# Optimization experiments

Hardware: AMD Instinct MI355X
Metric: run time of the kernel (lower is better)

Reference implementation:

```python
import jax, jax.numpy as jnp
import numpy as np

# dims: batch, time points, control channels (input_path_dim+1), cde state, mlp width
B, T, C, S, H = 64, 256, 16, 64, 128

# Tsit5 explicit tableau (5th-order solution weights; FSAL 7th stage has b7=0 and is skipped)
A21 = 0.161
A31, A32 = -0.008480655492356989, 0.335480655492357
A41, A42, A43 = 2.8971530571054935, -6.359448489975075, 4.3622954328695815
A51, A52, A53, A54 = 5.325864828439257, -11.748883564062828, 7.4955393428898365, -0.09249506636175525
A61, A62, A63, A64, A65 = 5.86145544294642, -12.92096931784711, 8.159367898576159, -0.071584973281401, -0.028269050394068383
C2, C3, C4, C5 = 0.161, 0.327, 0.9, 0.9800255409045097
BW = (0.09646076681806523, 0.01, 0.4798896504144996, 1.379008574103742, -3.290069515436081, 2.324710524099774)


def _mlp(x, ws, bs, final_act):
    for w, b in zip(ws[:-1], bs[:-1]):
        x = jax.nn.softplus(x @ w.T + b)
    return final_act(x @ ws[-1].T + bs[-1])


def _from_6d(v):  # (..., 6) -> (..., 3, 3) via Gram-Schmidt (Zhou et al. 6D rotation rep)
    a1, a2 = v[..., :3], v[..., 3:]
    b1 = a1 / jnp.linalg.norm(a1, axis=-1, keepdims=True)
    a2p = a2 - jnp.sum(b1 * a2, axis=-1, keepdims=True) * b1
    b2 = a2p / jnp.linalg.norm(a2p, axis=-1, keepdims=True)
    b3 = jnp.cross(b1, b2)
    return jnp.stack([b1, b2, b3], axis=-1)


def setup_inputs() -> dict:
    key = jax.random.key(0)
    ks = jax.random.split(key, 8)

    def lin(k, fan_in, fan_out):  # equinox Linear init: U(-1/sqrt(in), 1/sqrt(in))
        k1, k2 = jax.random.split(k)
        lim = 1.0 / np.sqrt(fan_in)
        w = jax.random.uniform(k1, (fan_out, fan_in), minval=-lim, maxval=lim, dtype=jnp.float32)
        b = jax.random.uniform(k2, (fan_out,), minval=-lim, maxval=lim, dtype=jnp.float32)
        return w, b

    ic_w0, ic_b0 = lin(ks[0], C, H)
    ic_w1, ic_b1 = lin(ks[1], H, H)
    ic_w2, ic_b2 = lin(ks[2], H, S)
    vf_w0, vf_b0 = lin(ks[3], S, H)
    vf_w1, vf_b1 = lin(ks[4], H, H)
    vf_w2, vf_b2 = lin(ks[5], H, S * C)
    ro_w, ro_b = lin(ks[6], S, 6)
    control_values = jax.random.normal(ks[7], (B, T, C), dtype=jnp.float32)
    return dict(control_values=control_values,
                ic_w0=ic_w0, ic_b0=ic_b0, ic_w1=ic_w1, ic_b1=ic_b1, ic_w2=ic_w2, ic_b2=ic_b2,
                vf_w0=vf_w0, vf_b0=vf_b0, vf_w1=vf_w1, vf_b1=vf_b1, vf_w2=vf_w2, vf_b2=vf_b2,
                ro_w=ro_w, ro_b=ro_b)


def reference(control_values, ic_w0, ic_b0, ic_w1, ic_b1, ic_w2, ic_b2,
              vf_w0, vf_b0, vf_w1, vf_b1, vf_w2, vf_b2, ro_w, ro_b):
    b, t, c = control_values.shape
    s = ic_w2.shape[0]
    h = 1.0 / (t - 1)  # uniform ts = linspace(0, 1, T)
    xs = control_values
    # backward-Hermite derivatives: d[i] = (x[i]-x[i-1])/h, d[0] = d[1]
    d = jnp.diff(xs, axis=1) / h                       # (B, T-1, C)
    dfull = jnp.concatenate([d[:, :1], d], axis=1)     # (B, T, C)

    ic_ws, ic_bs = [ic_w0, ic_w1, ic_w2], [ic_b0, ic_b1, ic_b2]
    vf_ws, vf_bs = [vf_w0, vf_w1, vf_w2], [vf_b0, vf_b1, vf_b2]

    y0 = _mlp(xs[:, 0], ic_ws, ic_bs, lambda x: x)     # (B, S)

    def vf_mat(y):  # (B, S) -> (B, S, C)
        return _mlp(y, vf_ws, vf_bs, jnp.tanh).reshape(b, s, c)

    def step(y, iv):
        yi, yip1, di, dip1 = iv  # each (B, C): interval endpoints & Hermite derivs

        def dXdt(sc):  # derivative of cubic Hermite at local coord sc in [0,1]
            s2 = sc * sc
            return (((6 * s2 - 6 * sc) / h) * yi + (3 * s2 - 4 * sc + 1) * di
                    + ((6 * sc - 6 * s2) / h) * yip1 + (3 * s2 - 2 * sc) * dip1)

        def f(yy, sc):
            return jnp.einsum('bsc,bc->bs', vf_mat(yy), dXdt(sc))

        k1 = f(y, 0.0)
        k2 = f(y + h * (A21 * k1), C2)
        k3 = f(y + h * (A31 * k1 + A32 * k2), C3)
        k4 = f(y + h * (A41 * k1 + A42 * k2 + A43 * k3), C4)
        k5 = f(y + h * (A51 * k1 + A52 * k2 + A53 * k3 + A54 * k4), C5)
        k6 = f(y + h * (A61 * k1 + A62 * k2 + A63 * k3 + A64 * k4 + A65 * k5), 1.0)
        yn = y + h * (BW[0] * k1 + BW[1] * k2 + BW[2] * k3 + BW[3] * k4 + BW[4] * k5 + BW[5] * k6)
        return yn, yn

    ivs = (jnp.swapaxes(xs[:, :-1], 0, 1), jnp.swapaxes(xs[:, 1:], 0, 1),
           jnp.swapaxes(dfull[:, :-1], 0, 1), jnp.swapaxes(dfull[:, 1:], 0, 1))
    _, ys = jax.lax.scan(step, y0, ivs)                # (T-1, B, S)
    hidden = jnp.swapaxes(jnp.concatenate([y0[None], ys], axis=0), 0, 1)  # (B, T, S)

    out6 = hidden @ ro_w.T + ro_b                      # (B, T, 6); identity readout activation
    return _from_6d(out6)                              # (B, T, 3, 3)
```

## Files before the change

### kernel.cpp

```cpp
#include <hip/hip_runtime.h>


typedef float float4v __attribute__((ext_vector_type(4)));
typedef float float2v __attribute__((ext_vector_type(2)));

__device__ __forceinline__ float dot4(float4v a, float4v b) {
  return a.x * b.x + a.y * b.y + a.z * b.z + a.w * b.w;
}

__device__ __forceinline__ float softplus_fast(float x) {
  float z = __expf(-fabsf(x));
  return fmaxf(x, 0.f) + __logf(1.f + z);
}

__device__ __forceinline__ float tanh_hw(float x) {
  float e = __expf(2.f * x);
  return 1.f - 2.f * __builtin_amdgcn_rcpf(e + 1.f);
}

__global__ __attribute__((amdgpu_waves_per_eu(2, 2)))
__launch_bounds__(512, 1) void cde_main(
    const float* __restrict__ xs,
    const float* __restrict__ icw0, const float* __restrict__ icb0,
    const float* __restrict__ icw1, const float* __restrict__ icb1,
    const float* __restrict__ icw2, const float* __restrict__ icb2,
    const float* __restrict__ vfw0, const float* __restrict__ vfb0,
    const float* __restrict__ vfw1, const float* __restrict__ vfb1,
    const float* __restrict__ vfw2, const float* __restrict__ vfb2,
    float* __restrict__ ybuf) {
  constexpr float Ac[6][5] = {
      {0.f, 0.f, 0.f, 0.f, 0.f},
      {0.161f, 0.f, 0.f, 0.f, 0.f},
      {-0.008480655492356989f, 0.335480655492357f, 0.f, 0.f, 0.f},
      {2.8971530571054935f, -6.359448489975075f, 4.3622954328695815f, 0.f, 0.f},
      {5.325864828439257f, -11.748883564062828f, 7.4955393428898365f,
       -0.09249506636175525f, 0.f},
      {5.86145544294642f, -12.92096931784711f, 8.159367898576159f,
       -0.071584973281401f, -0.028269050394068383f}};
  constexpr float SCv[6] = {0.f, 0.161f, 0.327f, 0.9f, 0.9800255409045097f, 1.f};
  constexpr float BWv[6] = {0.09646076681806523f, 0.01f, 0.4798896504144996f,
                            1.379008574103742f, -3.290069515436081f,
                            2.324710524099774f};

  const int tid = threadIdx.x;
  const int w = tid >> 6, l = tid & 63;
  const int b = blockIdx.x;

  __shared__ float sW2t[38][1024];
  __shared__ __align__(16) float sYtw[8][64];
  __shared__ __align__(16) float sH1[128];
  __shared__ __align__(16) float sH2[128];
  __shared__ float sK[6][64];

  for (int i = tid; i < 38 * 1024; i += 512) {
    int k = i >> 10, r = i & 1023;
    sW2t[k][r] = vfw2[(size_t)r * 128 + 90 + k];
  }

  const int r0 = tid * 2, r1 = r0 + 1;
  float w2a[72], w2b[72];
  {
    const float4v* p0 = (const float4v*)(vfw2 + (size_t)r0 * 128);
    const float4v* p1 = (const float4v*)(vfw2 + (size_t)r1 * 128);
#pragma unroll
    for (int kk = 0; kk < 18; ++kk) {
      float4v a = p0[kk], c = p1[kk];
      w2a[4 * kk + 0] = a.x; w2a[4 * kk + 1] = a.y;
      w2a[4 * kk + 2] = a.z; w2a[4 * kk + 3] = a.w;
      w2b[4 * kk + 0] = c.x; w2b[4 * kk + 1] = c.y;
      w2b[4 * kk + 2] = c.z; w2b[4 * kk + 3] = c.w;
    }
  }
#pragma unroll
  for (int kk = 0; kk < 72; ++kk)
    asm volatile("" : "+v"(w2a[kk]), "+v"(w2b[kk]));

  const int ii = tid >> 2, q4 = tid & 3;
  float w0r[16], w1r[32];
  {
    const float4v* p = (const float4v*)(vfw0 + (size_t)ii * 64 + q4 * 16);
#pragma unroll
    for (int kk = 0; kk < 4; ++kk) {
      float4v a = p[kk];
      w0r[4 * kk] = a.x; w0r[4 * kk + 1] = a.y;
      w0r[4 * kk + 2] = a.z; w0r[4 * kk + 3] = a.w;
    }
  }
  {
    const float4v* p = (const float4v*)(vfw1 + (size_t)ii * 128 + q4 * 32);
#pragma unroll
    for (int kk = 0; kk < 8; ++kk) {
      float4v a = p[kk];
      w1r[4 * kk] = a.x; w1r[4 * kk + 1] = a.y;
      w1r[4 * kk + 2] = a.z; w1r[4 * kk + 3] = a.w;
    }
  }
#pragma unroll
  for (int kk = 0; kk < 16; ++kk) asm volatile("" : "+v"(w0r[kk]));
#pragma unroll
  for (int kk = 0; kk < 32; ++kk) asm volatile("" : "+v"(w1r[kk]));

  const float b2r0 = vfb2[r0], b2r1 = vfb2[r1];
  const int c0 = (2 * l) & 15;
  const float b0i = vfb0[ii], b1i = vfb1[ii];

  const float* Xb = xs + (size_t)b * 4096;
  float* yb = ybuf + (size_t)b * 16384;

  __syncthreads();

  float* sTA = &sK[0][0];
  float* sTB = sH1;
  if (tid < 128) {
    float a = icb0[tid];
    const float* wr = icw0 + tid * 16;
#pragma unroll
    for (int k = 0; k < 16; ++k) a += wr[k] * Xb[k];
    sTA[tid] = softplus_fast(a);
  }
  __syncthreads();
  if (tid < 128) {
    float a = icb1[tid];
    const float* wr = icw1 + tid * 128;
    for (int k = 0; k < 128; ++k) a += wr[k] * sTA[k];
    sTB[tid] = softplus_fast(a);
  }
  __syncthreads();
  if (tid < 64) {
    float a = icb2[tid];
    const float* wr = icw2 + tid * 128;
    for (int k = 0; k < 128; ++k) a += wr[k] * sTB[k];
    sH2[tid] = a;
  }
  __syncthreads();
  float yreg = sH2[l];
  if (w == 0) yb[l] = yreg;

  const float hstep = 1.f / 255.f;
  const float invh = 255.f;

#pragma unroll 1
  for (int t = 0; t < 255; ++t) {
    float2v xt = *(const float2v*)(Xb + t * 16 + c0);
    float2v xt1 = *(const float2v*)(Xb + (t + 1) * 16 + c0);
    float2v xtm = xt;
    if (t != 0) xtm = *(const float2v*)(Xb + (t - 1) * 16 + c0);
    const float u0 = xt.x - xt1.x, u1 = xt.y - xt1.y;
    const float dp0 = (xt1.x - xt.x) * invh;
    const float dp1 = (xt1.y - xt.y) * invh;
    float di0 = (t == 0) ? dp0 : (xt.x - xtm.x) * invh;
    float di1 = (t == 0) ? dp1 : (xt.y - xtm.y) * invh;
#pragma unroll 1
    for (int j = 0; j < 6; ++j) {
      const float* wr0 = vfw2 + (size_t)r0 * 128;
      const float* wr1 = vfw2 + (size_t)r1 * 128;
      float4v sa0 = *(const float4v*)(wr0 + 72);
      float4v sa1 = *(const float4v*)(wr0 + 76);
      float4v sa2 = *(const float4v*)(wr0 + 80);
      float4v sa3 = *(const float4v*)(wr0 + 84);
      float2v sa4 = *(const float2v*)(wr0 + 88);
      float4v sb0 = *(const float4v*)(wr1 + 72);
      float4v sb1 = *(const float4v*)(wr1 + 76);
      float4v sb2 = *(const float4v*)(wr1 + 80);
      float4v sb3 = *(const float4v*)(wr1 + 84);
      float2v sb4 = *(const float2v*)(wr1 + 88);
      {
        float yt = yreg;
#pragma unroll
        for (int m = 0; m < 5; ++m)
          if (m < j) yt += hstep * Ac[j][m] * sK[m][l];
        sYtw[w][l] = yt;
      }
      asm volatile("s_waitcnt lgkmcnt(0)" ::: "memory");
      const float sc = SCv[j], s2 = sc * sc;
      const float a1 = (6.f * s2 - 6.f * sc) * invh;
      const float a2 = 3.f * s2 - 4.f * sc + 1.f;
      const float a3 = 3.f * s2 - 2.f * sc;
      const float dx0 = a1 * u0 + a2 * di0 + a3 * dp0;
      const float dx1 = a1 * u1 + a2 * di1 + a3 * dp1;
      {
        const float4v* yv = (const float4v*)(&sYtw[w][0] + q4 * 16);
        float4v y0 = yv[0], y1 = yv[1], y2 = yv[2], y3 = yv[3];
        float s = w0r[0] * y0.x + w0r[1] * y0.y + w0r[2] * y0.z +
                  w0r[3] * y0.w + w0r[4] * y1.x + w0r[5] * y1.y +
                  w0r[6] * y1.z + w0r[7] * y1.w + w0r[8] * y2.x +
                  w0r[9] * y2.y + w0r[10] * y2.z + w0r[11] * y2.w +
                  w0r[12] * y3.x + w0r[13] * y3.y + w0r[14] * y3.z +
                  w0r[15] * y3.w;
        s += __shfl_xor(s, 1);
        s += __shfl_xor(s, 2);
        if (q4 == 0) sH1[ii] = softplus_fast(s + b0i);
      }
      __syncthreads();
      {
        const float4v* hv = (const float4v*)(sH1 + q4 * 32);
        float s = 0.f;
#pragma unroll
        for (int kk = 0; kk < 8; ++kk) {
          float4v h = hv[kk];
          s += w1r[4 * kk] * h.x + w1r[4 * kk + 1] * h.y +
               w1r[4 * kk + 2] * h.z + w1r[4 * kk + 3] * h.w;
        }
        s += __shfl_xor(s, 1);
        s += __shfl_xor(s, 2);
        if (q4 == 0) sH2[ii] = softplus_fast(s + b1i);
      }
      __syncthreads();
      {
        const float4v* hv = (const float4v*)sH2;
        float s0 = 0.f, s1 = 0.f;
#pragma unroll
        for (int kk = 0; kk < 18; ++kk) {
          float4v h = hv[kk];
          s0 += w2a[4 * kk] * h.x + w2a[4 * kk + 1] * h.y +
                w2a[4 * kk + 2] * h.z + w2a[4 * kk + 3] * h.w;
          s1 += w2b[4 * kk] * h.x + w2b[4 * kk + 1] * h.y +
                w2b[4 * kk + 2] * h.z + w2b[4 * kk + 3] * h.w;
        }
        {
          float4v h0 = hv[18], h1 = hv[19], h2 = hv[20], h3 = hv[21];
          float2v h4 = *(const float2v*)(sH2 + 88);
          s0 += dot4(sa0, h0) + dot4(sa1, h1) + dot4(sa2, h2) +
                dot4(sa3, h3) + sa4.x * h4.x + sa4.y * h4.y;
          s1 += dot4(sb0, h0) + dot4(sb1, h1) + dot4(sb2, h2) +
                dot4(sb3, h3) + sb4.x * h4.x + sb4.y * h4.y;
        }
#pragma unroll 4
        for (int k2 = 0; k2 < 19; ++k2) {
          float2v hk = *(const float2v*)(sH2 + 90 + 2 * k2);
          float2v wlo = *(const float2v*)&sW2t[2 * k2][r0];
          float2v whi = *(const float2v*)&sW2t[2 * k2 + 1][r0];
          s0 += wlo.x * hk.x + whi.x * hk.y;
          s1 += wlo.y * hk.x + whi.y * hk.y;
        }
        float f = tanh_hw(s0 + b2r0) * dx0 + tanh_hw(s1 + b2r1) * dx1;
        f += __shfl_xor(f, 1);
        f += __shfl_xor(f, 2);
        f += __shfl_xor(f, 4);
        if ((tid & 7) == 0) sK[j][tid >> 3] = f;
      }
      __syncthreads();
    }
    {
      float yn = yreg;
#pragma unroll
      for (int m = 0; m < 6; ++m) yn += hstep * BWv[m] * sK[m][l];
      yreg = yn;
      if (w == 0) yb[(size_t)(t + 1) * 64 + l] = yn;
    }
  }
}

__global__ __launch_bounds__(256) void readout(
    const float* __restrict__ ybuf, const float* __restrict__ row,
    const float* __restrict__ rob, float* __restrict__ out) {
  int idx = blockIdx.x * blockDim.x + threadIdx.x;
  const float* y = ybuf + (size_t)idx * 64;
  float p[6];
#pragma unroll
  for (int o = 0; o < 6; ++o) {
    const float4v* rr = (const float4v*)(row + o * 64);
    const float4v* yv = (const float4v*)y;
    float s = 0.f;
#pragma unroll
    for (int k = 0; k < 16; ++k) s += dot4(rr[k], yv[k]);
    p[o] = s + rob[o];
  }
  float a1x = p[0], a1y = p[1], a1z = p[2];
  float a2x = p[3], a2y = p[4], a2z = p[5];
  float n1 = rsqrtf(a1x * a1x + a1y * a1y + a1z * a1z);
  float b1x = a1x * n1, b1y = a1y * n1, b1z = a1z * n1;
  float d = b1x * a2x + b1y * a2y + b1z * a2z;
  float px = a2x - d * b1x, py = a2y - d * b1y, pz = a2z - d * b1z;
  float n2 = rsqrtf(px * px + py * py + pz * pz);
  float b2x = px * n2, b2y = py * n2, b2z = pz * n2;
  float b3x = b1y * b2z - b1z * b2y;
  float b3y = b1z * b2x - b1x * b2z;
  float b3z = b1x * b2y - b1y * b2x;
  float* o = out + (size_t)idx * 9;
  o[0] = b1x; o[1] = b2x; o[2] = b3x;
  o[3] = b1y; o[4] = b2y; o[5] = b3y;
  o[6] = b1z; o[7] = b2z; o[8] = b3z;
}

extern "C" void kernel_launch(void* const* d_in, const int* in_sizes, int n_in,
                              void* d_out, int out_size, void* d_ws,
                              size_t ws_size, hipStream_t stream) {
  (void)in_sizes; (void)n_in; (void)out_size; (void)ws_size;
  const float* xs   = (const float*)d_in[0];
  const float* icw0 = (const float*)d_in[1];
  const float* icb0 = (const float*)d_in[2];
  const float* icw1 = (const float*)d_in[3];
  const float* icb1 = (const float*)d_in[4];
  const float* icw2 = (const float*)d_in[5];
  const float* icb2 = (const float*)d_in[6];
  const float* vfw0 = (const float*)d_in[7];
  const float* vfb0 = (const float*)d_in[8];
  const float* vfw1 = (const float*)d_in[9];
  const float* vfb1 = (const float*)d_in[10];
  const float* vfw2 = (const float*)d_in[11];
  const float* vfb2 = (const float*)d_in[12];
  const float* row  = (const float*)d_in[13];
  const float* rob  = (const float*)d_in[14];
  float* ybuf = (float*)d_ws;

  hipLaunchKernelGGL(cde_main, dim3(64), dim3(512), 0, stream,
                     xs, icw0, icb0, icw1, icb1, icw2, icb2,
                     vfw0, vfb0, vfw1, vfb1, vfw2, vfb2, ybuf);
  hipLaunchKernelGGL(readout, dim3(64), dim3(256), 0, stream,
                     ybuf, row, rob, (float*)d_out);
}
```

Before: 6.526 ms.

## Pretranspose vf_w2 for coalesced spill reloads and auto-select kernel register variant

Adds a prep kernel that writes a column-major copy of the last vector-field weight into workspace. The main kernel then fills its shared-memory slab from that copy with coalesced reads, and reloads the 18 per-row weight columns that do not fit in registers from it every stage as coalesced float2 loads instead of strided row reads. It also compiles three variants of the kernel with different register-allocation attributes and picks one at first call from the reported scratch use and register count. The cost is an extra launch and workspace use, and the chosen variant depends on what the compiler reports.

After: 14.14 ms. 117% more time.

```diff
diff --git a/kernel.cpp b/kernel.cpp
--- a/kernel.cpp
+++ b/kernel.cpp
@@ -18,8 +18,7 @@
   return 1.f - 2.f * __builtin_amdgcn_rcpf(e + 1.f);
 }
 
-__global__ __attribute__((amdgpu_waves_per_eu(2, 2)))
-__launch_bounds__(512, 1) void cde_main(
+__device__ __forceinline__ void cde_body(
     const float* __restrict__ xs,
     const float* __restrict__ icw0, const float* __restrict__ icb0,
     const float* __restrict__ icw1, const float* __restrict__ icb1,
@@ -27,7 +26,7 @@
     const float* __restrict__ vfw0, const float* __restrict__ vfb0,
     const float* __restrict__ vfw1, const float* __restrict__ vfb1,
     const float* __restrict__ vfw2, const float* __restrict__ vfb2,
-    float* __restrict__ ybuf) {
+    const float* __restrict__ w2t, float* __restrict__ ybuf) {
   constexpr float Ac[6][5] = {
       {0.f, 0.f, 0.f, 0.f, 0.f},
       {0.161f, 0.f, 0.f, 0.f, 0.f},
@@ -52,9 +51,16 @@
   __shared__ __align__(16) float sH2[128];
   __shared__ float sK[6][64];
 
-  for (int i = tid; i < 38 * 1024; i += 512) {
-    int k = i >> 10, r = i & 1023;
-    sW2t[k][r] = vfw2[(size_t)r * 128 + 90 + k];
+  if (w2t) {
+    for (int i = tid; i < 38 * 1024; i += 512) {
+      int k = i >> 10, r = i & 1023;
+      sW2t[k][r] = w2t[(size_t)(90 + k) * 1024 + r];
+    }
+  } else {
+    for (int i = tid; i < 38 * 1024; i += 512) {
+      int k = i >> 10, r = i & 1023;
+      sW2t[k][r] = vfw2[(size_t)r * 128 + 90 + k];
+    }
   }
 
   const int r0 = tid * 2, r1 = r0 + 1;
@@ -152,18 +158,21 @@
     float di1 = (t == 0) ? dp1 : (xt.y - xtm.y) * invh;
 #pragma unroll 1
     for (int j = 0; j < 6; ++j) {
-      const float* wr0 = vfw2 + (size_t)r0 * 128;
-      const float* wr1 = vfw2 + (size_t)r1 * 128;
-      float4v sa0 = *(const float4v*)(wr0 + 72);
-      float4v sa1 = *(const float4v*)(wr0 + 76);
-      float4v sa2 = *(const float4v*)(wr0 + 80);
-      float4v sa3 = *(const float4v*)(wr0 + 84);
-      float2v sa4 = *(const float2v*)(wr0 + 88);
-      float4v sb0 = *(const float4v*)(wr1 + 72);
-      float4v sb1 = *(const float4v*)(wr1 + 76);
-      float4v sb2 = *(const float4v*)(wr1 + 80);
-      float4v sb3 = *(const float4v*)(wr1 + 84);
-      float2v sb4 = *(const float2v*)(wr1 + 88);
+      float2v st[18];
+      if (w2t) {
+        const float* sbase = w2t + (size_t)72 * 1024 + r0;
+#pragma unroll
+        for (int c = 0; c < 18; ++c)
+          st[c] = *(const float2v*)(sbase + (size_t)c * 1024);
+      } else {
+        const float* wr0 = vfw2 + (size_t)r0 * 128;
+        const float* wr1 = vfw2 + (size_t)r1 * 128;
+#pragma unroll
+        for (int c = 0; c < 18; ++c) {
+          st[c].x = wr0[72 + c];
+          st[c].y = wr1[72 + c];
+        }
+      }
       {
         float yt = yreg;
 #pragma unroll
@@ -218,12 +227,20 @@
                 w2b[4 * kk + 2] * h.z + w2b[4 * kk + 3] * h.w;
         }
         {
-          float4v h0 = hv[18], h1 = hv[19], h2 = hv[20], h3 = hv[21];
+          float4v h0 = hv[18], h1 = hv[19], h2f = hv[20], h3 = hv[21];
           float2v h4 = *(const float2v*)(sH2 + 88);
-          s0 += dot4(sa0, h0) + dot4(sa1, h1) + dot4(sa2, h2) +
-                dot4(sa3, h3) + sa4.x * h4.x + sa4.y * h4.y;
-          s1 += dot4(sb0, h0) + dot4(sb1, h1) + dot4(sb2, h2) +
-                dot4(sb3, h3) + sb4.x * h4.x + sb4.y * h4.y;
+          s0 += st[0].x * h0.x + st[1].x * h0.y + st[2].x * h0.z +
+                st[3].x * h0.w + st[4].x * h1.x + st[5].x * h1.y +
+                st[6].x * h1.z + st[7].x * h1.w + st[8].x * h2f.x +
+                st[9].x * h2f.y + st[10].x * h2f.z + st[11].x * h2f.w +
+                st[12].x * h3.x + st[13].x * h3.y + st[14].x * h3.z +
+                st[15].x * h3.w + st[16].x * h4.x + st[17].x * h4.y;
+          s1 += st[0].y * h0.x + st[1].y * h0.y + st[2].y * h0.z +
+                st[3].y * h0.w + st[4].y * h1.x + st[5].y * h1.y +
+                st[6].y * h1.z + st[7].y * h1.w + st[8].y * h2f.x +
+                st[9].y * h2f.y + st[10].y * h2f.z + st[11].y * h2f.w +
+                st[12].y * h3.x + st[13].y * h3.y + st[14].y * h3.z +
+                st[15].y * h3.w + st[16].y * h4.x + st[17].y * h4.y;
         }
 #pragma unroll 4
         for (int k2 = 0; k2 < 19; ++k2) {
@@ -249,6 +266,39 @@
       if (w == 0) yb[(size_t)(t + 1) * 64 + l] = yn;
     }
   }
+}
+
+#define CDE_ARGS_DECL \
+    const float* __restrict__ xs, \
+    const float* __restrict__ icw0, const float* __restrict__ icb0, \
+    const float* __restrict__ icw1, const float* __restrict__ icb1, \
+    const float* __restrict__ icw2, const float* __restrict__ icb2, \
+    const float* __restrict__ vfw0, const float* __restrict__ vfb0, \
+    const float* __restrict__ vfw1, const float* __restrict__ vfb1, \
+    const float* __restrict__ vfw2, const float* __restrict__ vfb2, \
+    const float* __restrict__ w2t, float* __restrict__ ybuf
+#define CDE_ARGS_PASS \
+    xs, icw0, icb0, icw1, icb1, icw2, icb2, vfw0, vfb0, vfw1, vfb1, vfw2, \
+    vfb2, w2t, ybuf
+
+__global__ __attribute__((amdgpu_flat_work_group_size(512, 512),
+                          amdgpu_waves_per_eu(2, 2)))
+void cde_wpe(CDE_ARGS_DECL) { cde_body(CDE_ARGS_PASS); }
+
+__global__ __attribute__((amdgpu_flat_work_group_size(512, 512),
+                          amdgpu_num_vgpr(256)))
+void cde_nvg(CDE_ARGS_DECL) { cde_body(CDE_ARGS_PASS); }
+
+__global__ __attribute__((amdgpu_waves_per_eu(2, 2)))
+__launch_bounds__(512, 1) void cde_base(CDE_ARGS_DECL) {
+  cde_body(CDE_ARGS_PASS);
+}
+
+__global__ __launch_bounds__(256) void w2t_prep(const float* __restrict__ w2,
+                                                float* __restrict__ out) {
+  int i = blockIdx.x * 256 + threadIdx.x;
+  int r = i >> 7, c = i & 127;
+  out[(size_t)c * 1024 + r] = w2[i];
 }
 
 __global__ __launch_bounds__(256) void readout(
@@ -286,7 +336,7 @@
 extern "C" void kernel_launch(void* const* d_in, const int* in_sizes, int n_in,
                               void* d_out, int out_size, void* d_ws,
                               size_t ws_size, hipStream_t stream) {
-  (void)in_sizes; (void)n_in; (void)out_size; (void)ws_size;
+  (void)in_sizes; (void)n_in; (void)out_size;
   const float* xs   = (const float*)d_in[0];
   const float* icw0 = (const float*)d_in[1];
   const float* icb0 = (const float*)d_in[2];
@@ -303,10 +353,43 @@
   const float* row  = (const float*)d_in[13];
   const float* rob  = (const float*)d_in[14];
   float* ybuf = (float*)d_ws;
-
-  hipLaunchKernelGGL(cde_main, dim3(64), dim3(512), 0, stream,
-                     xs, icw0, icb0, icw1, icb1, icw2, icb2,
-                     vfw0, vfb0, vfw1, vfb1, vfw2, vfb2, ybuf);
+  float* w2t = nullptr;
+  if (ws_size >= (size_t)(4u * 1024u * 1024u + 512u * 1024u))
+    w2t = (float*)d_ws + 1048576;
+
+  static int pick = -1;
+  if (pick < 0) {
+    const void* fns[3] = {(const void*)cde_wpe, (const void*)cde_nvg,
+                          (const void*)cde_base};
+    long best = -0x7fffffffL;
+    for (int i = 0; i < 3; ++i) {
+      hipFuncAttributes fa{};
+      if (hipFuncGetAttributes(&fa, fns[i]) != hipSuccess) continue;
+      long score = -(long)fa.localSizeBytes * 4096 + (long)fa.numRegs;
+      if (score > best) { best = score; pick = i; }
+    }
+    if (pick < 0) pick = 2;
+  }
+
+  if (w2t)
+    hipLaunchKernelGGL(w2t_prep, dim3(512), dim3(256), 0, stream, vfw2, w2t);
+
+  if (pick == 0)
+    hipLaunchKernelGGL(cde_wpe, dim3(64), dim3(512), 0, stream,
+                       xs, icw0, icb0, icw1, icb1, icw2, icb2,
+                       vfw0, vfb0, vfw1, vfb1, vfw2, vfb2,
+                       (const float*)w2t, ybuf);
+  else if (pick == 1)
+    hipLaunchKernelGGL(cde_nvg, dim3(64), dim3(512), 0, stream,
+                       xs, icw0, icb0, icw1, icb1, icw2, icb2,
+                       vfw0, vfb0, vfw1, vfb1, vfw2, vfb2,
+                       (const float*)w2t, ybuf);
+  else
+    hipLaunchKernelGGL(cde_base, dim3(64), dim3(512), 0, stream,
+                       xs, icw0, icb0, icw1, icb1, icw2, icb2,
+                       vfw0, vfb0, vfw1, vfb1, vfw2, vfb2,
+                       (const float*)w2t, ybuf);
+
   hipLaunchKernelGGL(readout, dim3(64), dim3(256), 0, stream,
                      ybuf, row, rob, (float*)d_out);
 }
```

## Stream vf_w2 from a repacked interleaved buffer instead of register caching

Applied to the files above, without the earlier changes.

Removes the 144 per-thread registers that cached the first 72 columns of the last vector-field layer weights. Those weights and the previously per-stage global loads of columns 72-89 are now read from global memory on every stage. A small prep kernel repacks vf_w2 into a column-pair-major layout so each thread's two rows come in as a coalesced float4 per column pair. This lowers register pressure at the cost of much more global/L2 traffic inside the serial time loop. The old row-major path is kept as a fallback when the workspace is too small.

Result: slower. 9.955 ms (+52.5%).

```diff
diff --git a/kernel.cpp b/kernel.cpp
--- a/kernel.cpp
+++ b/kernel.cpp
@@ -18,8 +18,8 @@
   return 1.f - 2.f * __builtin_amdgcn_rcpf(e + 1.f);
 }
 
-__global__ __attribute__((amdgpu_waves_per_eu(2, 2)))
-__launch_bounds__(512, 1) void cde_main(
+template <bool USEP>
+__device__ __forceinline__ void cde_body(
     const float* __restrict__ xs,
     const float* __restrict__ icw0, const float* __restrict__ icb0,
     const float* __restrict__ icw1, const float* __restrict__ icb1,
@@ -27,7 +27,7 @@
     const float* __restrict__ vfw0, const float* __restrict__ vfb0,
     const float* __restrict__ vfw1, const float* __restrict__ vfb1,
     const float* __restrict__ vfw2, const float* __restrict__ vfb2,
-    float* __restrict__ ybuf) {
+    const float* __restrict__ w2p, float* __restrict__ ybuf) {
   constexpr float Ac[6][5] = {
       {0.f, 0.f, 0.f, 0.f, 0.f},
       {0.161f, 0.f, 0.f, 0.f, 0.f},
@@ -52,29 +52,20 @@
   __shared__ __align__(16) float sH2[128];
   __shared__ float sK[6][64];
 
-  for (int i = tid; i < 38 * 1024; i += 512) {
-    int k = i >> 10, r = i & 1023;
-    sW2t[k][r] = vfw2[(size_t)r * 128 + 90 + k];
+  if (USEP) {
+    for (int i = tid; i < 38 * 1024; i += 512) {
+      int k = i >> 10, r = i & 1023;
+      int c = 90 + k;
+      sW2t[k][r] = w2p[(size_t)(c >> 1) * 2048 + r * 2 + (c & 1)];
+    }
+  } else {
+    for (int i = tid; i < 38 * 1024; i += 512) {
+      int k = i >> 10, r = i & 1023;
+      sW2t[k][r] = vfw2[(size_t)r * 128 + 90 + k];
+    }
   }
 
   const int r0 = tid * 2, r1 = r0 + 1;
-  float w2a[72], w2b[72];
-  {
-    const float4v* p0 = (const float4v*)(vfw2 + (size_t)r0 * 128);
-    const float4v* p1 = (const float4v*)(vfw2 + (size_t)r1 * 128);
-#pragma unroll
-    for (int kk = 0; kk < 18; ++kk) {
-      float4v a = p0[kk], c = p1[kk];
-      w2a[4 * kk + 0] = a.x; w2a[4 * kk + 1] = a.y;
-      w2a[4 * kk + 2] = a.z; w2a[4 * kk + 3] = a.w;
-      w2b[4 * kk + 0] = c.x; w2b[4 * kk + 1] = c.y;
-      w2b[4 * kk + 2] = c.z; w2b[4 * kk + 3] = c.w;
-    }
-  }
-#pragma unroll
-  for (int kk = 0; kk < 72; ++kk)
-    asm volatile("" : "+v"(w2a[kk]), "+v"(w2b[kk]));
-
   const int ii = tid >> 2, q4 = tid & 3;
   float w0r[16], w1r[32];
   {
@@ -152,18 +143,6 @@
     float di1 = (t == 0) ? dp1 : (xt.y - xtm.y) * invh;
 #pragma unroll 1
     for (int j = 0; j < 6; ++j) {
-      const float* wr0 = vfw2 + (size_t)r0 * 128;
-      const float* wr1 = vfw2 + (size_t)r1 * 128;
-      float4v sa0 = *(const float4v*)(wr0 + 72);
-      float4v sa1 = *(const float4v*)(wr0 + 76);
-      float4v sa2 = *(const float4v*)(wr0 + 80);
-      float4v sa3 = *(const float4v*)(wr0 + 84);
-      float2v sa4 = *(const float2v*)(wr0 + 88);
-      float4v sb0 = *(const float4v*)(wr1 + 72);
-      float4v sb1 = *(const float4v*)(wr1 + 76);
-      float4v sb2 = *(const float4v*)(wr1 + 80);
-      float4v sb3 = *(const float4v*)(wr1 + 84);
-      float2v sb4 = *(const float2v*)(wr1 + 88);
       {
         float yt = yreg;
 #pragma unroll
@@ -207,23 +186,40 @@
       }
       __syncthreads();
       {
-        const float4v* hv = (const float4v*)sH2;
         float s0 = 0.f, s1 = 0.f;
-#pragma unroll
-        for (int kk = 0; kk < 18; ++kk) {
-          float4v h = hv[kk];
-          s0 += w2a[4 * kk] * h.x + w2a[4 * kk + 1] * h.y +
-                w2a[4 * kk + 2] * h.z + w2a[4 * kk + 3] * h.w;
-          s1 += w2b[4 * kk] * h.x + w2b[4 * kk + 1] * h.y +
-                w2b[4 * kk + 2] * h.z + w2b[4 * kk + 3] * h.w;
-        }
-        {
-          float4v h0 = hv[18], h1 = hv[19], h2 = hv[20], h3 = hv[21];
-          float2v h4 = *(const float2v*)(sH2 + 88);
-          s0 += dot4(sa0, h0) + dot4(sa1, h1) + dot4(sa2, h2) +
-                dot4(sa3, h3) + sa4.x * h4.x + sa4.y * h4.y;
-          s1 += dot4(sb0, h0) + dot4(sb1, h1) + dot4(sb2, h2) +
-                dot4(sb3, h3) + sb4.x * h4.x + sb4.y * h4.y;
+        if (USEP) {
+          const float* pb = w2p + (size_t)r0 * 2;
+#pragma unroll
+          for (int q = 0; q < 22; ++q) {
+            float4v h = *(const float4v*)(sH2 + 4 * q);
+            float4v wA = *(const float4v*)(pb + (size_t)(2 * q) * 2048);
+            float4v wB = *(const float4v*)(pb + (size_t)(2 * q + 1) * 2048);
+            s0 += wA.x * h.x + wA.y * h.y + wB.x * h.z + wB.y * h.w;
+            s1 += wA.z * h.x + wA.w * h.y + wB.z * h.z + wB.w * h.w;
+          }
+          {
+            float2v h = *(const float2v*)(sH2 + 88);
+            float4v wA = *(const float4v*)(pb + (size_t)44 * 2048);
+            s0 += wA.x * h.x + wA.y * h.y;
+            s1 += wA.z * h.x + wA.w * h.y;
+          }
+        } else {
+          const float* wr0 = vfw2 + (size_t)r0 * 128;
+          const float* wr1 = vfw2 + (size_t)r1 * 128;
+          const float4v* hv = (const float4v*)sH2;
+#pragma unroll
+          for (int kk = 0; kk < 22; ++kk) {
+            float4v h = hv[kk];
+            float4v a = ((const float4v*)wr0)[kk];
+            float4v c = ((const float4v*)wr1)[kk];
+            s0 += dot4(a, h);
+            s1 += dot4(c, h);
+          }
+          {
+            float2v h = *(const float2v*)(sH2 + 88);
+            s0 += wr0[88] * h.x + wr0[89] * h.y;
+            s1 += wr1[88] * h.x + wr1[89] * h.y;
+          }
         }
 #pragma unroll 4
         for (int k2 = 0; k2 < 19; ++k2) {
@@ -251,6 +247,35 @@
   }
 }
 
+#define CDE_ARGS_DECL \
+    const float* __restrict__ xs, \
+    const float* __restrict__ icw0, const float* __restrict__ icb0, \
+    const float* __restrict__ icw1, const float* __restrict__ icb1, \
+    const float* __restrict__ icw2, const float* __restrict__ icb2, \
+    const float* __restrict__ vfw0, const float* __restrict__ vfb0, \
+    const float* __restrict__ vfw1, const float* __restrict__ vfb1, \
+    const float* __restrict__ vfw2, const float* __restrict__ vfb2, \
+    const float* __restrict__ w2p, float* __restrict__ ybuf
+#define CDE_ARGS_PASS \
+    xs, icw0, icb0, icw1, icb1, icw2, icb2, vfw0, vfb0, vfw1, vfb1, vfw2, \
+    vfb2, w2p, ybuf
+
+__global__ __attribute__((amdgpu_waves_per_eu(2, 2)))
+__launch_bounds__(512, 1) void cde_p(CDE_ARGS_DECL) {
+  cde_body<true>(CDE_ARGS_PASS);
+}
+__global__ __attribute__((amdgpu_waves_per_eu(2, 2)))
+__launch_bounds__(512, 1) void cde_rm(CDE_ARGS_DECL) {
+  cde_body<false>(CDE_ARGS_PASS);
+}
+
+__global__ __launch_bounds__(256) void w2p_prep(const float* __restrict__ w2,
+                                                float* __restrict__ out) {
+  int i = blockIdx.x * 256 + threadIdx.x;
+  int r = i >> 7, c = i & 127;
+  out[(size_t)(c >> 1) * 2048 + r * 2 + (c & 1)] = w2[i];
+}
+
 __global__ __launch_bounds__(256) void readout(
     const float* __restrict__ ybuf, const float* __restrict__ row,
     const float* __restrict__ rob, float* __restrict__ out) {
@@ -286,7 +311,7 @@
 extern "C" void kernel_launch(void* const* d_in, const int* in_sizes, int n_in,
                               void* d_out, int out_size, void* d_ws,
                               size_t ws_size, hipStream_t stream) {
-  (void)in_sizes; (void)n_in; (void)out_size; (void)ws_size;
+  (void)in_sizes; (void)n_in; (void)out_size;
   const float* xs   = (const float*)d_in[0];
   const float* icw0 = (const float*)d_in[1];
   const float* icb0 = (const float*)d_in[2];
@@ -303,10 +328,23 @@
   const float* row  = (const float*)d_in[13];
   const float* rob  = (const float*)d_in[14];
   float* ybuf = (float*)d_ws;
-
-  hipLaunchKernelGGL(cde_main, dim3(64), dim3(512), 0, stream,
-                     xs, icw0, icb0, icw1, icb1, icw2, icb2,
-                     vfw0, vfb0, vfw1, vfb1, vfw2, vfb2, ybuf);
+  float* w2p = nullptr;
+  if (ws_size >= (size_t)(4u * 1024u * 1024u + 512u * 1024u))
+    w2p = (float*)d_ws + 1048576;
+
+  if (w2p) {
+    hipLaunchKernelGGL(w2p_prep, dim3(512), dim3(256), 0, stream, vfw2, w2p);
+    hipLaunchKernelGGL(cde_p, dim3(64), dim3(512), 0, stream,
+                       xs, icw0, icb0, icw1, icb1, icw2, icb2,
+                       vfw0, vfb0, vfw1, vfb1, vfw2, vfb2,
+                       (const float*)w2p, ybuf);
+  } else {
+    hipLaunchKernelGGL(cde_rm, dim3(64), dim3(512), 0, stream,
+                       xs, icw0, icb0, icw1, icb1, icw2, icb2,
+                       vfw0, vfb0, vfw1, vfb1, vfw2, vfb2,
+                       (const float*)nullptr, ybuf);
+  }
+
   hipLaunchKernelGGL(readout, dim3(64), dim3(256), 0, stream,
                      ybuf, row, rob, (float*)d_out);
 }
```

## Park vf_w2 weight columns in AGPRs and reload more columns per stage

Applied to the files above, without the earlier changes.

Moves the per-thread register cache of the first 64 vf_w2 columns (two rows) into accumulation VGPRs using explicit accvgpr write/read instructions, and shrinks it from 72 to 64 columns. Columns 64-89 are now reloaded from global memory each stage: 64-75 at stage start and 76-89 as a later load inside the matvec. The goal is to free architectural VGPRs and lower register pressure or spills. The cost is extra accvgpr_read instructions, more global/L1 loads per stage, and a second load whose latency may not be hidden. It also replaces the empty asm register pins with v_mov no-ops.

Result: slower. 11.70 ms (+79.3%).

```diff
diff --git a/kernel.cpp b/kernel.cpp
--- a/kernel.cpp
+++ b/kernel.cpp
@@ -17,6 +17,11 @@
   float e = __expf(2.f * x);
   return 1.f - 2.f * __builtin_amdgcn_rcpf(e + 1.f);
 }
+
+#define AG_WR(dst, src) \
+  asm volatile("v_accvgpr_write_b32 %0, %1" : "=a"(dst) : "v"(src))
+#define AG_RD(dst, src) \
+  asm volatile("v_accvgpr_read_b32 %0, %1" : "=v"(dst) : "a"(src))
 
 __global__ __attribute__((amdgpu_waves_per_eu(2, 2)))
 __launch_bounds__(512, 1) void cde_main(
@@ -58,22 +63,23 @@
   }
 
   const int r0 = tid * 2, r1 = r0 + 1;
-  float w2a[72], w2b[72];
+  float agA[64], agB[64];
   {
     const float4v* p0 = (const float4v*)(vfw2 + (size_t)r0 * 128);
     const float4v* p1 = (const float4v*)(vfw2 + (size_t)r1 * 128);
 #pragma unroll
-    for (int kk = 0; kk < 18; ++kk) {
+    for (int kk = 0; kk < 16; ++kk) {
       float4v a = p0[kk], c = p1[kk];
-      w2a[4 * kk + 0] = a.x; w2a[4 * kk + 1] = a.y;
-      w2a[4 * kk + 2] = a.z; w2a[4 * kk + 3] = a.w;
-      w2b[4 * kk + 0] = c.x; w2b[4 * kk + 1] = c.y;
-      w2b[4 * kk + 2] = c.z; w2b[4 * kk + 3] = c.w;
-    }
-  }
-#pragma unroll
-  for (int kk = 0; kk < 72; ++kk)
-    asm volatile("" : "+v"(w2a[kk]), "+v"(w2b[kk]));
+      AG_WR(agA[4 * kk + 0], a.x);
+      AG_WR(agA[4 * kk + 1], a.y);
+      AG_WR(agA[4 * kk + 2], a.z);
+      AG_WR(agA[4 * kk + 3], a.w);
+      AG_WR(agB[4 * kk + 0], c.x);
+      AG_WR(agB[4 * kk + 1], c.y);
+      AG_WR(agB[4 * kk + 2], c.z);
+      AG_WR(agB[4 * kk + 3], c.w);
+    }
+  }
 
   const int ii = tid >> 2, q4 = tid & 3;
   float w0r[16], w1r[32];
@@ -96,9 +102,11 @@
     }
   }
 #pragma unroll
-  for (int kk = 0; kk < 16; ++kk) asm volatile("" : "+v"(w0r[kk]));
-#pragma unroll
-  for (int kk = 0; kk < 32; ++kk) asm volatile("" : "+v"(w1r[kk]));
+  for (int kk = 0; kk < 16; ++kk)
+    asm volatile("v_mov_b32 %0, %0" : "+v"(w0r[kk]));
+#pragma unroll
+  for (int kk = 0; kk < 32; ++kk)
+    asm volatile("v_mov_b32 %0, %0" : "+v"(w1r[kk]));
 
   const float b2r0 = vfb2[r0], b2r1 = vfb2[r1];
   const int c0 = (2 * l) & 15;
@@ -150,20 +158,16 @@
     const float dp1 = (xt1.y - xt.y) * invh;
     float di0 = (t == 0) ? dp0 : (xt.x - xtm.x) * invh;
     float di1 = (t == 0) ? dp1 : (xt.y - xtm.y) * invh;
+    const float* wr0 = vfw2 + (size_t)r0 * 128;
+    const float* wr1 = vfw2 + (size_t)r1 * 128;
 #pragma unroll 1
     for (int j = 0; j < 6; ++j) {
-      const float* wr0 = vfw2 + (size_t)r0 * 128;
-      const float* wr1 = vfw2 + (size_t)r1 * 128;
-      float4v sa0 = *(const float4v*)(wr0 + 72);
-      float4v sa1 = *(const float4v*)(wr0 + 76);
-      float4v sa2 = *(const float4v*)(wr0 + 80);
-      float4v sa3 = *(const float4v*)(wr0 + 84);
-      float2v sa4 = *(const float2v*)(wr0 + 88);
-      float4v sb0 = *(const float4v*)(wr1 + 72);
-      float4v sb1 = *(const float4v*)(wr1 + 76);
-      float4v sb2 = *(const float4v*)(wr1 + 80);
-      float4v sb3 = *(const float4v*)(wr1 + 84);
-      float2v sb4 = *(const float2v*)(wr1 + 88);
+      float4v sa0 = *(const float4v*)(wr0 + 64);
+      float4v sa1 = *(const float4v*)(wr0 + 68);
+      float4v sa2 = *(const float4v*)(wr0 + 72);
+      float4v sb0 = *(const float4v*)(wr1 + 64);
+      float4v sb1 = *(const float4v*)(wr1 + 68);
+      float4v sb2 = *(const float4v*)(wr1 + 72);
       {
         float yt = yreg;
 #pragma unroll
@@ -210,20 +214,40 @@
         const float4v* hv = (const float4v*)sH2;
         float s0 = 0.f, s1 = 0.f;
 #pragma unroll
-        for (int kk = 0; kk < 18; ++kk) {
+        for (int kk = 0; kk < 16; ++kk) {
           float4v h = hv[kk];
-          s0 += w2a[4 * kk] * h.x + w2a[4 * kk + 1] * h.y +
-                w2a[4 * kk + 2] * h.z + w2a[4 * kk + 3] * h.w;
-          s1 += w2b[4 * kk] * h.x + w2b[4 * kk + 1] * h.y +
-                w2b[4 * kk + 2] * h.z + w2b[4 * kk + 3] * h.w;
+          float a0_, a1_, a2_, a3_, c0_, c1_, c2_, c3_;
+          AG_RD(a0_, agA[4 * kk + 0]);
+          AG_RD(a1_, agA[4 * kk + 1]);
+          AG_RD(a2_, agA[4 * kk + 2]);
+          AG_RD(a3_, agA[4 * kk + 3]);
+          AG_RD(c0_, agB[4 * kk + 0]);
+          AG_RD(c1_, agB[4 * kk + 1]);
+          AG_RD(c2_, agB[4 * kk + 2]);
+          AG_RD(c3_, agB[4 * kk + 3]);
+          s0 += a0_ * h.x + a1_ * h.y + a2_ * h.z + a3_ * h.w;
+          s1 += c0_ * h.x + c1_ * h.y + c2_ * h.z + c3_ * h.w;
         }
         {
-          float4v h0 = hv[18], h1 = hv[19], h2 = hv[20], h3 = hv[21];
-          float2v h4 = *(const float2v*)(sH2 + 88);
-          s0 += dot4(sa0, h0) + dot4(sa1, h1) + dot4(sa2, h2) +
-                dot4(sa3, h3) + sa4.x * h4.x + sa4.y * h4.y;
-          s1 += dot4(sb0, h0) + dot4(sb1, h1) + dot4(sb2, h2) +
-                dot4(sb3, h3) + sb4.x * h4.x + sb4.y * h4.y;
+          float4v h0 = hv[16], h1 = hv[17], h2f = hv[18];
+          s0 += dot4(sa0, h0) + dot4(sa1, h1) + dot4(sa2, h2f);
+          s1 += dot4(sb0, h0) + dot4(sb1, h1) + dot4(sb2, h2f);
+        }
+        {
+          float4v ta0 = *(const float4v*)(wr0 + 76);
+          float4v ta1 = *(const float4v*)(wr0 + 80);
+          float4v ta2 = *(const float4v*)(wr0 + 84);
+          float2v ta3 = *(const float2v*)(wr0 + 88);
+          float4v tb0 = *(const float4v*)(wr1 + 76);
+          float4v tb1 = *(const float4v*)(wr1 + 80);
+          float4v tb2 = *(const float4v*)(wr1 + 84);
+          float2v tb3 = *(const float2v*)(wr1 + 88);
+          float4v h0 = hv[19], h1 = hv[20], h2f = hv[21];
+          float2v h3 = *(const float2v*)(sH2 + 88);
+          s0 += dot4(ta0, h0) + dot4(ta1, h1) + dot4(ta2, h2f) +
+                ta3.x * h3.x + ta3.y * h3.y;
+          s1 += dot4(tb0, h0) + dot4(tb1, h1) + dot4(tb2, h2f) +
+                tb3.x * h3.x + tb3.y * h3.y;
         }
 #pragma unroll 4
         for (int k2 = 0; k2 < 19; ++k2) {
```
